# Optimization experiments

Measured on AMD Instinct MI355X. Metric: run time of the kernel, lower is better.

Reference implementation:

```python
import jax, jax.numpy as jnp
import numpy as np
from jax.ops import segment_sum

N = 100000      # nodes
E = 1600000     # edges
G = 128         # graphs in batch
D = 128         # input (embedding) dim
H = 128         # hidden dim
WALK = 16       # random-walk length
PED = 16        # PE embed dim
L = 5           # GNN layers
OUT = 10        # classes
EPS = 1e-5      # batchnorm eps


def setup_inputs() -> dict:
    key = jax.random.key(0)
    ks = jax.random.split(key, 32)
    f = lambda k, shp: (jax.random.normal(k, shp, dtype=jnp.float32) * 0.05)
    inp = {
        'x': jnp.zeros((N,), dtype=jnp.int64) if jax.config.jax_enable_x64 else jnp.zeros((N,), dtype=jnp.int32),
        'edge_index': jax.random.randint(ks[0], (2, E), 0, N),
        'batch': jnp.sort(jax.random.randint(ks[1], (N,), 0, G)),
        'emb_table': f(ks[2], (1, D)),
        'pe_w': f(ks[3], (WALK, PED)), 'pe_b': f(ks[4], (PED,)),
        'proj_w': f(ks[5], (D + PED, H)), 'proj_b': f(ks[6], (H,)),
        'gin_w1': f(ks[7], (L, H, H)), 'gin_b1': f(ks[8], (L, H)),
        'gin_w2': f(ks[9], (L, H, H)), 'gin_b2': f(ks[10], (L, H)),
        'bn_g': jnp.ones((L, H), jnp.float32), 'bn_b': jnp.zeros((L, H), jnp.float32),
        'ffn_w1': f(ks[11], (L, H, 2 * H)), 'ffn_b1': f(ks[12], (L, 2 * H)),
        'ffn_w2': f(ks[13], (L, 2 * H, H)), 'ffn_b2': f(ks[14], (L, H)),
        'ffn_bn_g': jnp.ones((L, H), jnp.float32), 'ffn_bn_b': jnp.zeros((L, H), jnp.float32),
        'out_w1': f(ks[15], (H, H)), 'out_b1': f(ks[16], (H,)),
        'out_w2': f(ks[17], (H, OUT)), 'out_b2': f(ks[18], (OUT,)),
    }
    return inp


def _batchnorm(h, g, b):
    # BatchNorm1d forward with batch statistics (training-mode math)
    mu = jnp.mean(h, axis=0)
    var = jnp.var(h, axis=0)
    return (h - mu) * jax.lax.rsqrt(var + EPS) * g + b


def _forward(emb_table, pe_w, pe_b, proj_w, proj_b, gin_w1, gin_b1, gin_w2, gin_b2,
             bn_g, bn_b, ffn_w1, ffn_b1, ffn_w2, ffn_b2, ffn_bn_g, ffn_bn_b,
             out_w1, out_b1, out_w2, out_b2, x, edge_index, batch):
    h0 = emb_table[x]                                # [N, D] (all indices are 0)

    # ---- RandomWalkPositionalEncoding (vectorized scatter-add per step) ----
    row0, col0 = edge_index[0], edge_index[1]
    loops = jnp.arange(N)
    row = jnp.concatenate([row0, loops])
    col = jnp.concatenate([col0, loops])             # self loops appended
    deg = segment_sum(jnp.ones(row.shape, jnp.float32), col, num_segments=N)
    dinv = jnp.where(deg > 0, jax.lax.rsqrt(jnp.maximum(deg, 1.0)), 0.0)
    norm_e = dinv[row] * dinv[col]                   # [E+N]

    cnt = segment_sum(jnp.ones((N,), jnp.float32), batch, num_segments=G)
    prob = 1.0 / jnp.maximum(cnt, 1.0)[batch]        # per-graph uniform init

    def rw_step(p, _):
        new_p = segment_sum(p[row] * norm_e, col, num_segments=N)
        return new_p * 0.9 + p * 0.1, p

    _, rw = jax.lax.scan(rw_step, prob, None, length=WALK)   # [WALK, N]
    pe = rw.T @ pe_w + pe_b                          # [N, PED]

    # ---- input projection ----
    h = jnp.concatenate([h0, pe], axis=-1) @ proj_w + proj_b # [N, H]

    # ---- stacked GIN layers with BN, residual and FFN (dropout = eval identity) ----
    for i in range(L):
        res = h
        agg = segment_sum(h[row0], col0, num_segments=N) + h  # GIN: (1+eps)x + sum_j x_j, eps=0
        z = jax.nn.relu(agg @ gin_w1[i] + gin_b1[i]) @ gin_w2[i] + gin_b2[i]
        z = jax.nn.relu(_batchnorm(z, bn_g[i], bn_b[i]))
        h = z + res
        res2 = h
        f = jax.nn.relu(h @ ffn_w1[i] + ffn_b1[i]) @ ffn_w2[i] + ffn_b2[i]
        h = _batchnorm(f + res2, ffn_bn_g[i], ffn_bn_b[i])

    # ---- global mean pooling + MLP head ----
    gsum = segment_sum(h, batch, num_segments=G)
    g = gsum / jnp.maximum(cnt, 1.0)[:, None]        # [G, H]
    out = jax.nn.relu(g @ out_w1 + out_b1) @ out_w2 + out_b2
    return out                                        # [G, OUT]


def reference(x, edge_index, batch, emb_table, pe_w, pe_b, proj_w, proj_b,
              gin_w1, gin_b1, gin_w2, gin_b2, bn_g, bn_b, ffn_w1, ffn_b1,
              ffn_w2, ffn_b2, ffn_bn_g, ffn_bn_b, out_w1, out_b1, out_w2, out_b2):
    return _forward(emb_table, pe_w, pe_b, proj_w, proj_b, gin_w1, gin_b1, gin_w2,
                    gin_b2, bn_g, bn_b, ffn_w1, ffn_b1, ffn_w2, ffn_b2,
                    ffn_bn_g, ffn_bn_b, out_w1, out_b1, out_w2, out_b2,
                    x, edge_index, batch)
```

## Files before the change

kernel.cpp:

```cpp
#include <hip/hip_runtime.h>
#include <math.h>

#define NN 100000
#define NE 1600000
#define NG 128
#define HD 128
#define WLK 16
#define NL 5
#define NOUT 10
#define BNEPS 1e-5f
#define CDIV(a,b) (((a)+(b)-1)/(b))

#define NBKT 782
#define NEB 400
#define EPB 4000
#define NSCAN (NBKT*NEB)
#define NSB CDIV(NSCAN,1024)
#define NBM 782

typedef float f32x4 __attribute__((ext_vector_type(4)));
typedef _Float16 f16x8 __attribute__((ext_vector_type(8)));
typedef unsigned short ushort_t;
typedef unsigned int uint_t;

__device__ __forceinline__ ushort_t f2h(float x) {
    union { _Float16 h; ushort_t u; } c;
    c.h = (_Float16)x;
    return c.u;
}
__device__ __forceinline__ float h2f(ushort_t u) {
    union { ushort_t u; _Float16 h; } c;
    c.u = u;
    return (float)c.h;
}

__global__ void k_cnt(const int* __restrict__ batch, int* __restrict__ cnt,
                      int* __restrict__ goff) {
    int g = threadIdx.x;
    if (g >= NG) return;
    int lo0 = 0, hi0 = NN;
    while (lo0 < hi0) { int m = (lo0 + hi0) >> 1; if (batch[m] < g) lo0 = m + 1; else hi0 = m; }
    int lo1 = lo0, hi1 = NN;
    while (lo1 < hi1) { int m = (lo1 + hi1) >> 1; if (batch[m] < g + 1) lo1 = m + 1; else hi1 = m; }
    cnt[g] = lo1 - lo0;
    goff[g] = lo0;
}

__global__ void k_bhist(const int* __restrict__ col0, int* __restrict__ bhist) {
    __shared__ int hist[NBKT];
    for (int i = threadIdx.x; i < NBKT; i += 256) hist[i] = 0;
    __syncthreads();
    int e0 = blockIdx.x * EPB;
    for (int e = e0 + threadIdx.x; e < e0 + EPB; e += 256) atomicAdd(&hist[col0[e] >> 7], 1);
    __syncthreads();
    for (int i = threadIdx.x; i < NBKT; i += 256) bhist[i * NEB + blockIdx.x] = hist[i];
}

__global__ void k_gscan1(const int* __restrict__ in, int* __restrict__ bsum) {
    __shared__ int sm[256];
    int base = blockIdx.x * 1024 + threadIdx.x * 4;
    int s = 0;
#pragma unroll
    for (int i = 0; i < 4; ++i) { int e = base + i; if (e < NSCAN) s += in[e]; }
    sm[threadIdx.x] = s; __syncthreads();
    for (int st = 128; st > 0; st >>= 1) {
        if (threadIdx.x < st) sm[threadIdx.x] += sm[threadIdx.x + st];
        __syncthreads();
    }
    if (threadIdx.x == 0) bsum[blockIdx.x] = sm[0];
}

__global__ void k_scan2(int* __restrict__ blksum, int nblk) {
    __shared__ int sm[512];
    int t = threadIdx.x;
    int x = (t < nblk) ? blksum[t] : 0;
    sm[t] = x; __syncthreads();
    for (int s = 1; s < 512; s <<= 1) {
        int v = (t >= s) ? sm[t - s] : 0;
        __syncthreads();
        sm[t] += v;
        __syncthreads();
    }
    if (t < nblk) blksum[t] = sm[t] - x;
}

__global__ void k_gscan3(const int* __restrict__ in, const int* __restrict__ bsum,
                         int* __restrict__ out) {
    __shared__ int sm[256];
    int t = threadIdx.x;
    int base = blockIdx.x * 1024 + t * 4;
    int v[4]; int s = 0;
#pragma unroll
    for (int i = 0; i < 4; ++i) { int e = base + i; v[i] = (e < NSCAN) ? in[e] : 0; s += v[i]; }
    sm[t] = s; __syncthreads();
    for (int st = 1; st < 256; st <<= 1) {
        int x = (t >= st) ? sm[t - st] : 0;
        __syncthreads();
        sm[t] += x;
        __syncthreads();
    }
    int excl = sm[t] - s + bsum[blockIdx.x];
#pragma unroll
    for (int i = 0; i < 4; ++i) { int e = base + i; if (e < NSCAN) { out[e] = excl; excl += v[i]; } }
}

__global__ void k_escatter(const int* __restrict__ row0, const int* __restrict__ col0,
                           const int* __restrict__ boffs, int2* __restrict__ epair) {
    __shared__ int cur[NBKT];
    for (int i = threadIdx.x; i < NBKT; i += 256) cur[i] = boffs[i * NEB + blockIdx.x];
    __syncthreads();
    int e0 = blockIdx.x * EPB;
    for (int e = e0 + threadIdx.x; e < e0 + EPB; e += 256) {
        int c = col0[e], r = row0[e];
        int pos = atomicAdd(&cur[c >> 7], 1);
        epair[pos] = make_int2(c, r);
    }
}

__global__ void k_bucket(const int2* __restrict__ epair, const int* __restrict__ boffs,
                         int* __restrict__ rowptr, int* __restrict__ deg,
                         int* __restrict__ esrc) {
    __shared__ int cnt_[128], scn[128], cur_[128];
    int bkt = blockIdx.x, t = threadIdx.x;
    int bs = boffs[bkt * NEB];
    int be = (bkt + 1 < NBKT) ? boffs[(bkt + 1) * NEB] : NE;
    if (t < 128) cnt_[t] = 0;
    __syncthreads();
    for (int e = bs + t; e < be; e += 256) atomicAdd(&cnt_[epair[e].x & 127], 1);
    __syncthreads();
    int c = (t < 128) ? cnt_[t] : 0;
    if (t < 128) scn[t] = c;
    __syncthreads();
    for (int st = 1; st < 128; st <<= 1) {
        int x = (t >= st && t < 128) ? scn[t - st] : 0;
        __syncthreads();
        if (t < 128) scn[t] += x;
        __syncthreads();
    }
    if (t < 128) {
        int excl = scn[t] - c;
        int node = bkt * 128 + t;
        if (node < NN) { rowptr[node] = bs + excl; deg[node] = c; }
        cur_[t] = bs + excl;
    }
    if (bkt == NBKT - 1 && t == 0) rowptr[NN] = NE;
    __syncthreads();
    for (int e = bs + t; e < be; e += 256) {
        int2 p = epair[e];
        int pos = atomicAdd(&cur_[p.x & 127], 1);
        esrc[pos] = p.y;
    }
}

__global__ void k_init_pe(const int* __restrict__ deg, const int* __restrict__ batch,
                          const int* __restrict__ cnt, float* __restrict__ dinv,
                          float* __restrict__ p, float* __restrict__ pd) {
    int v = blockIdx.x * 256 + threadIdx.x;
    if (v >= NN) return;
    float dv = rsqrtf((float)(deg[v] + 1));
    dinv[v] = dv;
    float pv = 1.0f / fmaxf((float)cnt[batch[v]], 1.0f);
    p[v] = pv; pd[v] = pv * dv;
}

__global__ void k_rw_step(const float* __restrict__ pin, const float* __restrict__ pdin,
                          const int* __restrict__ rowptr, const int* __restrict__ esrc,
                          const float* __restrict__ dinv, float* __restrict__ rwslice,
                          float* __restrict__ pout, float* __restrict__ pdout) {
    int v = blockIdx.x * 256 + threadIdx.x;
    if (v >= NN) return;
    int b = rowptr[v], e = rowptr[v + 1];
    float a[8];
#pragma unroll
    for (int k = 0; k < 8; ++k) a[k] = 0.f;
    int i = b;
    for (; i + 8 <= e; i += 8) {
        int s[8];
#pragma unroll
        for (int k = 0; k < 8; ++k) s[k] = esrc[i + k];
#pragma unroll
        for (int k = 0; k < 8; ++k) a[k] += pdin[s[k]];
    }
    for (; i < e; ++i) a[0] += pdin[esrc[i]];
    float s = ((a[0] + a[1]) + (a[2] + a[3])) + ((a[4] + a[5]) + (a[6] + a[7]));
    float dv = dinv[v];
    float pv = pin[v];
    float np = s * dv + pv * dv * dv;
    float nxt = 0.9f * np + 0.1f * pv;
    rwslice[v] = pv;
    pout[v] = nxt;
    pdout[v] = nxt * dv;
}

__global__ void k_mc1(const float* __restrict__ emb, const float* __restrict__ pe_w,
                      const float* __restrict__ pe_b, const float* __restrict__ proj_w,
                      const float* __restrict__ proj_b, float* __restrict__ M,
                      float* __restrict__ c1, float* __restrict__ bnA0,
                      float* __restrict__ bnB0) {
    int j = threadIdx.x;
    bnA0[j] = 1.f; bnB0[j] = 0.f;
    float c0 = proj_b[j];
    for (int d = 0; d < HD; ++d) c0 += emb[d] * proj_w[d * HD + j];
    for (int w = 0; w < WLK; ++w) c0 += pe_b[w] * proj_w[(HD + w) * HD + j];
    c1[j] = c0;
    for (int s = 0; s < WLK; ++s) {
        float m = 0.f;
        for (int w = 0; w < WLK; ++w) m += pe_w[s * WLK + w] * proj_w[(HD + w) * HD + j];
        M[s * HD + j] = m;
    }
}

__global__ void k_proj(const float* __restrict__ rw, const float* __restrict__ M,
                       const float* __restrict__ c1, uint2* __restrict__ th4) {
    int idx = blockIdx.x * 256 + threadIdx.x;
    if (idx >= NN * 32) return;
    int v = idx >> 5, cg = (idx & 31) * 4;
    float4 acc = *(const float4*)&c1[cg];
#pragma unroll
    for (int s = 0; s < WLK; ++s) {
        float r = rw[s * NN + v];
        float4 m = *(const float4*)&M[s * HD + cg];
        acc.x += r * m.x; acc.y += r * m.y; acc.z += r * m.z; acc.w += r * m.w;
    }
    th4[idx] = make_uint2((uint_t)f2h(acc.x) | ((uint_t)f2h(acc.y) << 16),
                          (uint_t)f2h(acc.z) | ((uint_t)f2h(acc.w) << 16));
}

__global__ void k_prepw(const float* __restrict__ g1, const float* __restrict__ g2,
                        const float* __restrict__ f1, const float* __restrict__ f2,
                        ushort_t* __restrict__ wt1, ushort_t* __restrict__ wt2,
                        ushort_t* __restrict__ wt3, ushort_t* __restrict__ wt4) {
    int i = blockIdx.x * 256 + threadIdx.x;
    if (i < 81920) {
        int l = i >> 14, rem = i & 16383, n = rem >> 7, k = rem & 127;
        wt1[i] = f2h(g1[l * 16384 + k * 128 + n]);
    } else if (i < 163840) {
        int j = i - 81920;
        int l = j >> 14, rem = j & 16383, n = rem >> 7, k = rem & 127;
        wt2[j] = f2h(g2[l * 16384 + k * 128 + n]);
    } else if (i < 327680) {
        int j = i - 163840;
        int l = j >> 15, rem = j & 32767, n = rem >> 7, k = rem & 127;
        wt3[j] = f2h(f1[l * 32768 + k * 256 + n]);
    } else {
        int j = i - 327680;
        int l = j >> 15, rem = j & 32767, n = rem >> 8, k = rem & 255;
        wt4[j] = f2h(f2[l * 32768 + k * 128 + n]);
    }
}

__global__ void k_aggb(const uint_t* __restrict__ th2, const int* __restrict__ rowptr,
                       const int* __restrict__ esrc, const float* __restrict__ bnA0,
                       const float* __restrict__ bnB0, uint_t* __restrict__ aggb2) {
    int wave = threadIdx.x >> 6, lane = threadIdx.x & 63;
    int v = blockIdx.x * 4 + wave;
    if (v >= NN) return;
    uint_t u = th2[(size_t)v * 64 + lane];
    float sx[8], sy[8];
#pragma unroll
    for (int k = 0; k < 8; ++k) { sx[k] = 0.f; sy[k] = 0.f; }
    sx[0] = h2f((ushort_t)(u & 0xFFFFu)); sy[0] = h2f((ushort_t)(u >> 16));
    int b = rowptr[v], e = rowptr[v + 1];
    int i = b;
    for (; i + 8 <= e; i += 8) {
        int idx[8]; uint_t x[8];
#pragma unroll
        for (int k = 0; k < 8; ++k) idx[k] = esrc[i + k];
#pragma unroll
        for (int k = 0; k < 8; ++k) x[k] = th2[(size_t)idx[k] * 64 + lane];
#pragma unroll
        for (int k = 0; k < 8; ++k) {
            sx[k] += h2f((ushort_t)(x[k] & 0xFFFFu));
            sy[k] += h2f((ushort_t)(x[k] >> 16));
        }
    }
    for (; i < e; ++i) {
        uint_t x = th2[(size_t)esrc[i] * 64 + lane];
        sx[0] += h2f((ushort_t)(x & 0xFFFFu)); sy[0] += h2f((ushort_t)(x >> 16));
    }
    float fx = ((sx[0] + sx[1]) + (sx[2] + sx[3])) + ((sx[4] + sx[5]) + (sx[6] + sx[7]));
    float fy = ((sy[0] + sy[1]) + (sy[2] + sy[3])) + ((sy[4] + sy[5]) + (sy[6] + sy[7]));
    float2 A = *(const float2*)&bnA0[lane * 2];
    float2 B = *(const float2*)&bnB0[lane * 2];
    float cf = (float)(e - b + 1);
    float ox = A.x * fx + cf * B.x;
    float oy = A.y * fy + cf * B.y;
    aggb2[(size_t)v * 64 + lane] = (uint_t)f2h(ox) | ((uint_t)f2h(oy) << 16);
}

#define GLDK 136
__global__ __launch_bounds__(256)
void k_gin(const ushort_t* __restrict__ A, const ushort_t* __restrict__ W1T,
           const ushort_t* __restrict__ W2T, const float* __restrict__ b1,
           const float* __restrict__ b2, ushort_t* __restrict__ z2h,
           float* __restrict__ partS, float* __restrict__ partQ) {
    __shared__ ushort_t As[128 * GLDK];
    __shared__ ushort_t Ws[64 * GLDK];
    __shared__ float sS[128], sQ[128];
    const int tid = threadIdx.x;
    const int w = tid >> 6, l = tid & 63;
    const int lm = l & 15, lq = l >> 4;
    const int rw0 = w * 32;
    const int vr0 = blockIdx.x * 128;
    if (tid < 128) { sS[tid] = 0.f; sQ[tid] = 0.f; }

#pragma unroll
    for (int it = 0; it < 8; ++it) {
        int f = it * 256 + tid;
        int row = f >> 4, sl = f & 15;
        uint4 a = make_uint4(0, 0, 0, 0);
        int vr = vr0 + row;
        if (vr < NN) a = *(const uint4*)&A[(size_t)vr * HD + sl * 8];
        *(uint4*)&As[row * GLDK + sl * 8] = a;
    }

    f32x4 z1a[2][2][4] = {};
    for (int c = 0; c < 2; ++c) {
        __syncthreads();
#pragma unroll
        for (int it = 0; it < 4; ++it) {
            int f = it * 256 + tid;
            int row = f >> 4, sl = f & 15;
            *(uint4*)&Ws[row * GLDK + sl * 8] =
                *(const uint4*)&W1T[(size_t)(c * 64 + row) * HD + sl * 8];
        }
        __syncthreads();
#pragma unroll
        for (int kk = 0; kk < 128; kk += 32) {
            f16x8 af[2], bf[4];
#pragma unroll
            for (int i = 0; i < 2; ++i)
                af[i] = *(const f16x8*)&As[(rw0 + i * 16 + lm) * GLDK + kk + lq * 8];
#pragma unroll
            for (int j = 0; j < 4; ++j)
                bf[j] = *(const f16x8*)&Ws[(j * 16 + lm) * GLDK + kk + lq * 8];
#pragma unroll
            for (int i = 0; i < 2; ++i)
#pragma unroll
                for (int j = 0; j < 4; ++j)
                    z1a[c][i][j] = __builtin_amdgcn_mfma_f32_16x16x32_f16(af[i], bf[j], z1a[c][i][j], 0, 0, 0);
        }
    }
    __syncthreads();

#pragma unroll
    for (int c = 0; c < 2; ++c)
#pragma unroll
        for (int j = 0; j < 4; ++j) {
            int col = c * 64 + j * 16 + lm;
            float bj = b1[col];
#pragma unroll
            for (int i = 0; i < 2; ++i)
#pragma unroll
                for (int r = 0; r < 4; ++r) {
                    int row = rw0 + i * 16 + lq * 4 + r;
                    As[row * GLDK + col] = f2h(fmaxf(z1a[c][i][j][r] + bj, 0.f));
                }
        }

    f32x4 z2a[2][2][4] = {};
    for (int c2 = 0; c2 < 2; ++c2) {
        __syncthreads();
#pragma unroll
        for (int it = 0; it < 4; ++it) {
            int f = it * 256 + tid;
            int row = f >> 4, sl = f & 15;
            *(uint4*)&Ws[row * GLDK + sl * 8] =
                *(const uint4*)&W2T[(size_t)(c2 * 64 + row) * HD + sl * 8];
        }
        __syncthreads();
#pragma unroll
        for (int kk = 0; kk < 128; kk += 32) {
            f16x8 af[2], bf[4];
#pragma unroll
            for (int i = 0; i < 2; ++i)
                af[i] = *(const f16x8*)&As[(rw0 + i * 16 + lm) * GLDK + kk + lq * 8];
#pragma unroll
            for (int j = 0; j < 4; ++j)
                bf[j] = *(const f16x8*)&Ws[(j * 16 + lm) * GLDK + kk + lq * 8];
#pragma unroll
            for (int i = 0; i < 2; ++i)
#pragma unroll
                for (int j = 0; j < 4; ++j)
                    z2a[c2][i][j] = __builtin_amdgcn_mfma_f32_16x16x32_f16(af[i], bf[j], z2a[c2][i][j], 0, 0, 0);
        }
    }

    float ls[2][4] = {}, lsq[2][4] = {};
#pragma unroll
    for (int c2 = 0; c2 < 2; ++c2)
#pragma unroll
        for (int j = 0; j < 4; ++j) {
            int col = c2 * 64 + j * 16 + lm;
            float bj = b2[col];
#pragma unroll
            for (int i = 0; i < 2; ++i)
#pragma unroll
                for (int r = 0; r < 4; ++r) {
                    int vr = vr0 + rw0 + i * 16 + lq * 4 + r;
                    if (vr < NN) {
                        float x = z2a[c2][i][j][r] + bj;
                        ls[c2][j] += x; lsq[c2][j] += x * x;
                        z2h[(size_t)vr * HD + col] = f2h(x);
                    }
                }
        }
#pragma unroll
    for (int c2 = 0; c2 < 2; ++c2)
#pragma unroll
        for (int j = 0; j < 4; ++j) {
            atomicAdd(&sS[c2 * 64 + j * 16 + lm], ls[c2][j]);
            atomicAdd(&sQ[c2 * 64 + j * 16 + lm], lsq[c2][j]);
        }
    __syncthreads();
    if (tid < 128) {
        partS[(size_t)tid * NBM + blockIdx.x] = sS[tid];
        partQ[(size_t)tid * NBM + blockIdx.x] = sQ[tid];
    }
}

__global__ __launch_bounds__(256)
void k_ffn1(const ushort_t* __restrict__ th, const ushort_t* __restrict__ z2h,
            const ushort_t* __restrict__ W3T, const float* __restrict__ b3,
            const float* __restrict__ bnA0, const float* __restrict__ bnB0,
            const float* __restrict__ bnA1, const float* __restrict__ bnB1,
            ushort_t* __restrict__ f1h) {
    __shared__ ushort_t As[128 * GLDK];
    __shared__ ushort_t Ws[64 * GLDK];
    __shared__ float sA0[128], sB0[128], sA1[128], sB1[128];
    const int tid = threadIdx.x;
    const int w = tid >> 6, l = tid & 63;
    const int lm = l & 15, lq = l >> 4;
    const int rw0 = w * 32;
    const int vr0 = blockIdx.x * 128;

    if (tid < 128) {
        sA0[tid] = bnA0[tid]; sB0[tid] = bnB0[tid];
        sA1[tid] = bnA1[tid]; sB1[tid] = bnB1[tid];
    }
    __syncthreads();

#pragma unroll
    for (int it = 0; it < 8; ++it) {
        int f = it * 256 + tid;
        int row = f >> 4, sl = f & 15;
        int vr = vr0 + row;
        uint4 o = make_uint4(0, 0, 0, 0);
        if (vr < NN) {
            uint4 tv = *(const uint4*)&th[(size_t)vr * HD + sl * 8];
            uint4 zv = *(const uint4*)&z2h[(size_t)vr * HD + sl * 8];
            uint_t tu[4] = {tv.x, tv.y, tv.z, tv.w};
            uint_t zu[4] = {zv.x, zv.y, zv.z, zv.w};
            uint_t ou[4];
#pragma unroll
            for (int m = 0; m < 4; ++m) {
                int ch0 = sl * 8 + m * 2;
                float t0 = h2f((ushort_t)(tu[m] & 0xFFFFu));
                float t1 = h2f((ushort_t)(tu[m] >> 16));
                float z0 = h2f((ushort_t)(zu[m] & 0xFFFFu));
                float z1 = h2f((ushort_t)(zu[m] >> 16));
                float h0 = sA0[ch0] * t0 + sB0[ch0] + fmaxf(sA1[ch0] * z0 + sB1[ch0], 0.f);
                float h1 = sA0[ch0 + 1] * t1 + sB0[ch0 + 1] + fmaxf(sA1[ch0 + 1] * z1 + sB1[ch0 + 1], 0.f);
                ou[m] = (uint_t)f2h(h0) | ((uint_t)f2h(h1) << 16);
            }
            o = make_uint4(ou[0], ou[1], ou[2], ou[3]);
        }
        *(uint4*)&As[row * GLDK + sl * 8] = o;
    }

    for (int c = 0; c < 4; ++c) {
        __syncthreads();
#pragma unroll
        for (int it = 0; it < 4; ++it) {
            int f = it * 256 + tid;
            int row = f >> 4, sl = f & 15;
            *(uint4*)&Ws[row * GLDK + sl * 8] =
                *(const uint4*)&W3T[(size_t)(c * 64 + row) * HD + sl * 8];
        }
        __syncthreads();
        f32x4 acc[2][4] = {};
#pragma unroll
        for (int kk = 0; kk < 128; kk += 32) {
            f16x8 af[2], bf[4];
#pragma unroll
            for (int i = 0; i < 2; ++i)
                af[i] = *(const f16x8*)&As[(rw0 + i * 16 + lm) * GLDK + kk + lq * 8];
#pragma unroll
            for (int j = 0; j < 4; ++j)
                bf[j] = *(const f16x8*)&Ws[(j * 16 + lm) * GLDK + kk + lq * 8];
#pragma unroll
            for (int i = 0; i < 2; ++i)
#pragma unroll
                for (int j = 0; j < 4; ++j)
                    acc[i][j] = __builtin_amdgcn_mfma_f32_16x16x32_f16(af[i], bf[j], acc[i][j], 0, 0, 0);
        }
#pragma unroll
        for (int j = 0; j < 4; ++j) {
            int col = c * 64 + j * 16 + lm;
            float bj = b3[col];
#pragma unroll
            for (int i = 0; i < 2; ++i)
#pragma unroll
                for (int r = 0; r < 4; ++r) {
                    int vr = vr0 + rw0 + i * 16 + lq * 4 + r;
                    if (vr < NN)
                        f1h[(size_t)vr * 256 + col] = f2h(fmaxf(acc[i][j][r] + bj, 0.f));
                }
        }
    }
}

__global__ __launch_bounds__(256, 2)
void k_ffn2(const ushort_t* __restrict__ f1h, const ushort_t* __restrict__ WT,
            const float* __restrict__ bias, ushort_t* __restrict__ th,
            const ushort_t* __restrict__ z2h,
            const float* __restrict__ bnA0, const float* __restrict__ bnB0,
            const float* __restrict__ bnA1, const float* __restrict__ bnB1,
            float* __restrict__ partS, float* __restrict__ partQ) {
    constexpr int LDK = 72;
    __shared__ ushort_t As[128 * LDK];
    __shared__ ushort_t Ws[128 * LDK];
    __shared__ float sS[128], sQ[128];
    const int tid = threadIdx.x;
    const int w = tid >> 6, l = tid & 63;
    const int lm = l & 15, lq = l >> 4;
    const int rb = (w >> 1) * 64, cbw = (w & 1) * 64;
    const int vr0 = blockIdx.x * 128;
    f32x4 acc[4][4] = {};

    for (int kt = 0; kt < 4; ++kt) {
        __syncthreads();
#pragma unroll
        for (int it = 0; it < 4; ++it) {
            int f = it * 256 + tid;
            int row = f >> 3, sl = f & 7;
            uint4 a = make_uint4(0, 0, 0, 0);
            int vr = vr0 + row;
            if (vr < NN) a = *(const uint4*)&f1h[(size_t)vr * 256 + kt * 64 + sl * 8];
            *(uint4*)&As[row * LDK + sl * 8] = a;
            uint4 wv = *(const uint4*)&WT[(size_t)row * 256 + kt * 64 + sl * 8];
            *(uint4*)&Ws[row * LDK + sl * 8] = wv;
        }
        __syncthreads();
#pragma unroll
        for (int kk = 0; kk < 64; kk += 32) {
            f16x8 af[4], bf[4];
#pragma unroll
            for (int i = 0; i < 4; ++i)
                af[i] = *(const f16x8*)&As[(rb + i * 16 + lm) * LDK + kk + lq * 8];
#pragma unroll
            for (int j = 0; j < 4; ++j)
                bf[j] = *(const f16x8*)&Ws[(cbw + j * 16 + lm) * LDK + kk + lq * 8];
#pragma unroll
            for (int i = 0; i < 4; ++i)
#pragma unroll
                for (int j = 0; j < 4; ++j)
                    acc[i][j] = __builtin_amdgcn_mfma_f32_16x16x32_f16(af[i], bf[j], acc[i][j], 0, 0, 0);
        }
    }

    float bcol[4], a0c[4], b0c[4], a1c[4], b1c[4];
#pragma unroll
    for (int j = 0; j < 4; ++j) {
        int c = cbw + j * 16 + lm;
        bcol[j] = bias[c];
        a0c[j] = bnA0[c]; b0c[j] = bnB0[c];
        a1c[j] = bnA1[c]; b1c[j] = bnB1[c];
    }
    if (tid < 128) { sS[tid] = 0.f; sQ[tid] = 0.f; }
    __syncthreads();
    float ls[4] = {0, 0, 0, 0}, lsq[4] = {0, 0, 0, 0};
#pragma unroll
    for (int i = 0; i < 4; ++i) {
#pragma unroll
        for (int r = 0; r < 4; ++r) {
            int vr = vr0 + rb + i * 16 + lq * 4 + r;
            if (vr < NN) {
#pragma unroll
                for (int j = 0; j < 4; ++j) {
                    int c = cbw + j * 16 + lm;
                    float t = h2f(th[(size_t)vr * HD + c]);
                    float z = h2f(z2h[(size_t)vr * HD + c]);
                    float resv = a0c[j] * t + b0c[j] + fmaxf(a1c[j] * z + b1c[j], 0.f);
                    float x = acc[i][j][r] + bcol[j] + resv;
                    ls[j] += x; lsq[j] += x * x;
                    th[(size_t)vr * HD + c] = f2h(x);
                }
            }
        }
    }
#pragma unroll
    for (int j = 0; j < 4; ++j) {
        atomicAdd(&sS[cbw + j * 16 + lm], ls[j]);
        atomicAdd(&sQ[cbw + j * 16 + lm], lsq[j]);
    }
    __syncthreads();
    if (tid < 128) {
        partS[(size_t)tid * NBM + blockIdx.x] = sS[tid];
        partQ[(size_t)tid * NBM + blockIdx.x] = sQ[tid];
    }
}

__global__ void k_bnparm(const float* __restrict__ partS, const float* __restrict__ partQ,
                         const float* __restrict__ g, const float* __restrict__ b,
                         float* __restrict__ bnA, float* __restrict__ bnB) {
    __shared__ float smS[256], smQ[256];
    int c = blockIdx.x, t = threadIdx.x;
    float s = 0.f, q = 0.f;
    for (int i = t; i < NBM; i += 256) {
        s += partS[(size_t)c * NBM + i];
        q += partQ[(size_t)c * NBM + i];
    }
    smS[t] = s; smQ[t] = q; __syncthreads();
    for (int st = 128; st > 0; st >>= 1) {
        if (t < st) { smS[t] += smS[t + st]; smQ[t] += smQ[t + st]; }
        __syncthreads();
    }
    if (t == 0) {
        float mu = smS[0] * (1.0f / NN);
        float var = smQ[0] * (1.0f / NN) - mu * mu;
        float inv = rsqrtf(var + BNEPS);
        float a = g[c] * inv;
        bnA[c] = a;
        bnB[c] = b[c] - mu * a;
    }
}

__global__ void k_pool(const uint2* __restrict__ th4, const int* __restrict__ goff,
                       const int* __restrict__ cnt, float* __restrict__ gsum) {
    __shared__ float4 sm[256];
    int g = blockIdx.x >> 2, sub = blockIdx.x & 3;
    int n0 = goff[g], n = cnt[g];
    int cg = threadIdx.x & 31, rl = threadIdx.x >> 5;
    float4 acc = make_float4(0.f, 0.f, 0.f, 0.f);
    for (int r = sub * 8 + rl; r < n; r += 32) {
        uint2 v = th4[(size_t)(n0 + r) * 32 + cg];
        acc.x += h2f((ushort_t)(v.x & 0xFFFFu));
        acc.y += h2f((ushort_t)(v.x >> 16));
        acc.z += h2f((ushort_t)(v.y & 0xFFFFu));
        acc.w += h2f((ushort_t)(v.y >> 16));
    }
    sm[threadIdx.x] = acc; __syncthreads();
    for (int st = 128; st >= 32; st >>= 1) {
        if (threadIdx.x < st) {
            float4 o = sm[threadIdx.x + st];
            sm[threadIdx.x].x += o.x; sm[threadIdx.x].y += o.y;
            sm[threadIdx.x].z += o.z; sm[threadIdx.x].w += o.w;
        }
        __syncthreads();
    }
    if (threadIdx.x < 32) {
        float4 v = sm[threadIdx.x];
        atomicAdd(&gsum[g * HD + cg * 4 + 0], v.x);
        atomicAdd(&gsum[g * HD + cg * 4 + 1], v.y);
        atomicAdd(&gsum[g * HD + cg * 4 + 2], v.z);
        atomicAdd(&gsum[g * HD + cg * 4 + 3], v.w);
    }
}

__global__ void k_head(const float* __restrict__ gsum, const int* __restrict__ cnt,
                       const float* __restrict__ bnA0, const float* __restrict__ bnB0,
                       const float* __restrict__ w1, const float* __restrict__ b1,
                       const float* __restrict__ w2, const float* __restrict__ b2,
                       float* __restrict__ out) {
    __shared__ float gv[HD], av[HD];
    int gid = blockIdx.x, t = threadIdx.x;
    float c = fmaxf((float)cnt[gid], 1.0f);
    gv[t] = bnA0[t] * (gsum[gid * HD + t] / c) + bnB0[t];
    __syncthreads();
    float a = b1[t];
    for (int k = 0; k < HD; ++k) a += gv[k] * w1[k * HD + t];
    av[t] = fmaxf(a, 0.f);
    __syncthreads();
    if (t < NOUT) {
        float o = b2[t];
        for (int k = 0; k < HD; ++k) o += av[k] * w2[k * NOUT + t];
        out[gid * NOUT + t] = o;
    }
}

static constexpr size_t AL(size_t x) { return (x + 511) & ~(size_t)511; }
static constexpr size_t OFF_TH     = 0;
static constexpr size_t OFF_SHARE  = OFF_TH     + AL((size_t)NN * HD * 2);
static constexpr size_t SZ_SHARE   = AL((size_t)NN * 256 * 2);
static constexpr size_t OFF_Z2     = OFF_SHARE  + SZ_SHARE;
static constexpr size_t OFF_RW     = OFF_Z2     + AL((size_t)NN * HD * 2);
static constexpr size_t OFF_P0     = OFF_RW     + AL((size_t)WLK * NN * 4);
static constexpr size_t OFF_P1     = OFF_P0     + AL((size_t)NN * 4);
static constexpr size_t OFF_PD0    = OFF_P1     + AL((size_t)NN * 4);
static constexpr size_t OFF_PD1    = OFF_PD0    + AL((size_t)NN * 4);
static constexpr size_t OFF_DINV   = OFF_PD1    + AL((size_t)NN * 4);
static constexpr size_t OFF_ESRC   = OFF_DINV   + AL((size_t)NN * 4);
static constexpr size_t OFF_ROWPTR = OFF_ESRC   + AL((size_t)NE * 4);
static constexpr size_t OFF_DEG    = OFF_ROWPTR + AL((size_t)(NN + 1) * 4);
static constexpr size_t OFF_BHIST  = OFF_DEG    + AL((size_t)NN * 4);
static constexpr size_t OFF_BOFFS  = OFF_BHIST  + AL((size_t)NSCAN * 4);
static constexpr size_t OFF_BSUM   = OFF_BOFFS  + AL((size_t)NSCAN * 4);
static constexpr size_t OFF_WT1    = OFF_BSUM   + AL(512 * 4);
static constexpr size_t OFF_WT2    = OFF_WT1    + AL((size_t)5 * 16384 * 2);
static constexpr size_t OFF_WT3    = OFF_WT2    + AL((size_t)5 * 16384 * 2);
static constexpr size_t OFF_WT4    = OFF_WT3    + AL((size_t)5 * 32768 * 2);
static constexpr size_t OFF_PARTS  = OFF_WT4    + AL((size_t)5 * 32768 * 2);
static constexpr size_t OFF_PARTQ  = OFF_PARTS  + AL((size_t)128 * NBM * 4);
static constexpr size_t OFF_BNA0   = OFF_PARTQ  + AL((size_t)128 * NBM * 4);
static constexpr size_t OFF_BNB0   = OFF_BNA0   + AL(128 * 4);
static constexpr size_t OFF_BNA1   = OFF_BNB0   + AL(128 * 4);
static constexpr size_t OFF_BNB1   = OFF_BNA1   + AL(128 * 4);
static constexpr size_t OFF_M      = OFF_BNB1   + AL(128 * 4);
static constexpr size_t OFF_C1     = OFF_M      + AL((size_t)WLK * HD * 4);
static constexpr size_t OFF_CNT    = OFF_C1     + AL(HD * 4);
static constexpr size_t OFF_GOFF   = OFF_CNT    + AL(NG * 4);
static constexpr size_t OFF_GSUM   = OFF_GOFF   + AL(NG * 4);
static constexpr size_t ZERO_BYTES = (size_t)NG * HD * 4;

extern "C" void kernel_launch(void* const* d_in, const int* in_sizes, int n_in,
                              void* d_out, int out_size, void* d_ws, size_t ws_size,
                              hipStream_t stream) {
    const int* eidx = (const int*)d_in[1];
    const int* row0 = eidx;
    const int* col0 = eidx + NE;
    const int* batch = (const int*)d_in[2];
    const float* emb = (const float*)d_in[3];
    const float* pe_w = (const float*)d_in[4];
    const float* pe_b = (const float*)d_in[5];
    const float* proj_w = (const float*)d_in[6];
    const float* proj_b = (const float*)d_in[7];
    const float* gin_w1 = (const float*)d_in[8];
    const float* gin_b1 = (const float*)d_in[9];
    const float* gin_w2 = (const float*)d_in[10];
    const float* gin_b2 = (const float*)d_in[11];
    const float* bn_g = (const float*)d_in[12];
    const float* bn_b = (const float*)d_in[13];
    const float* ffn_w1 = (const float*)d_in[14];
    const float* ffn_b1 = (const float*)d_in[15];
    const float* ffn_w2 = (const float*)d_in[16];
    const float* ffn_b2 = (const float*)d_in[17];
    const float* ffn_bn_g = (const float*)d_in[18];
    const float* ffn_bn_b = (const float*)d_in[19];
    const float* out_w1 = (const float*)d_in[20];
    const float* out_b1 = (const float*)d_in[21];
    const float* out_w2 = (const float*)d_in[22];
    const float* out_b2 = (const float*)d_in[23];
    float* out = (float*)d_out;

    char* ws = (char*)d_ws;
    ushort_t* th    = (ushort_t*)(ws + OFF_TH);
    ushort_t* aggh  = (ushort_t*)(ws + OFF_SHARE);
    ushort_t* f1h   = (ushort_t*)(ws + OFF_SHARE);
    int2*     epair = (int2*)(ws + OFF_SHARE);
    ushort_t* z2h   = (ushort_t*)(ws + OFF_Z2);
    float*    rw    = (float*)(ws + OFF_RW);
    float*    p0    = (float*)(ws + OFF_P0);
    float*    p1    = (float*)(ws + OFF_P1);
    float*    pd0   = (float*)(ws + OFF_PD0);
    float*    pd1   = (float*)(ws + OFF_PD1);
    float*    dinv  = (float*)(ws + OFF_DINV);
    int*      esrc  = (int*)(ws + OFF_ESRC);
    int*      rowptr= (int*)(ws + OFF_ROWPTR);
    int*      deg   = (int*)(ws + OFF_DEG);
    int*      bhist = (int*)(ws + OFF_BHIST);
    int*      boffs = (int*)(ws + OFF_BOFFS);
    int*      bsum  = (int*)(ws + OFF_BSUM);
    ushort_t* wt1   = (ushort_t*)(ws + OFF_WT1);
    ushort_t* wt2   = (ushort_t*)(ws + OFF_WT2);
    ushort_t* wt3   = (ushort_t*)(ws + OFF_WT3);
    ushort_t* wt4   = (ushort_t*)(ws + OFF_WT4);
    float*    partS = (float*)(ws + OFF_PARTS);
    float*    partQ = (float*)(ws + OFF_PARTQ);
    float*    bnA0  = (float*)(ws + OFF_BNA0);
    float*    bnB0  = (float*)(ws + OFF_BNB0);
    float*    bnA1  = (float*)(ws + OFF_BNA1);
    float*    bnB1  = (float*)(ws + OFF_BNB1);
    float*    M     = (float*)(ws + OFF_M);
    float*    c1    = (float*)(ws + OFF_C1);
    int*      cnt   = (int*)(ws + OFF_CNT);
    int*      goff  = (int*)(ws + OFF_GOFF);
    float*    gsum  = (float*)(ws + OFF_GSUM);

    const int NB = CDIV(NN, 256);
    const int NBV = CDIV(NN * 32, 256);

    hipMemsetAsync(ws + OFF_GSUM, 0, ZERO_BYTES, stream);

    k_cnt<<<1, 128, 0, stream>>>(batch, cnt, goff);
    k_bhist<<<NEB, 256, 0, stream>>>(col0, bhist);
    k_gscan1<<<NSB, 256, 0, stream>>>(bhist, bsum);
    k_scan2<<<1, 512, 0, stream>>>(bsum, NSB);
    k_gscan3<<<NSB, 256, 0, stream>>>(bhist, bsum, boffs);
    k_escatter<<<NEB, 256, 0, stream>>>(row0, col0, boffs, epair);
    k_bucket<<<NBKT, 256, 0, stream>>>(epair, boffs, rowptr, deg, esrc);

    k_init_pe<<<NB, 256, 0, stream>>>(deg, batch, cnt, dinv, p0, pd0);
    k_mc1<<<1, 128, 0, stream>>>(emb, pe_w, pe_b, proj_w, proj_b, M, c1, bnA0, bnB0);
    k_prepw<<<1920, 256, 0, stream>>>(gin_w1, gin_w2, ffn_w1, ffn_w2, wt1, wt2, wt3, wt4);
    for (int s = 0; s < WLK; ++s) {
        const float* pin = (s & 1) ? p1 : p0;
        const float* pdin = (s & 1) ? pd1 : pd0;
        float* pout = (s & 1) ? p0 : p1;
        float* pdout = (s & 1) ? pd0 : pd1;
        k_rw_step<<<NB, 256, 0, stream>>>(pin, pdin, rowptr, esrc, dinv,
                                          rw + (size_t)s * NN, pout, pdout);
    }
    k_proj<<<NBV, 256, 0, stream>>>(rw, M, c1, (uint2*)th);

    for (int i = 0; i < NL; ++i) {
        k_aggb<<<CDIV(NN, 4), 256, 0, stream>>>((const uint_t*)th, rowptr, esrc,
                                                bnA0, bnB0, (uint_t*)aggh);
        k_gin<<<NBM, 256, 0, stream>>>(aggh, wt1 + (size_t)i * 16384, wt2 + (size_t)i * 16384,
                                       gin_b1 + i * HD, gin_b2 + i * HD, z2h, partS, partQ);
        k_bnparm<<<128, 256, 0, stream>>>(partS, partQ, bn_g + i * HD, bn_b + i * HD, bnA1, bnB1);
        k_ffn1<<<NBM, 256, 0, stream>>>(th, z2h, wt3 + (size_t)i * 32768, ffn_b1 + i * 256,
                                        bnA0, bnB0, bnA1, bnB1, f1h);
        k_ffn2<<<NBM, 256, 0, stream>>>(f1h, wt4 + (size_t)i * 32768, ffn_b2 + i * HD,
                                        th, z2h, bnA0, bnB0, bnA1, bnB1, partS, partQ);
        k_bnparm<<<128, 256, 0, stream>>>(partS, partQ, ffn_bn_g + i * HD, ffn_bn_b + i * HD,
                                          bnA0, bnB0);
    }

    k_pool<<<NG * 4, 256, 0, stream>>>((const uint2*)th, goff, cnt, gsum);
    k_head<<<NG, 128, 0, stream>>>(gsum, cnt, bnA0, bnB0, out_w1, out_b1, out_w2, out_b2, out);
}
```

Before: 1.571 ms.

## Fuse FFN up- and down-projection into one kernel keeping hidden tile in LDS

```diff
diff --git a/kernel.cpp b/kernel.cpp
--- a/kernel.cpp
+++ b/kernel.cpp
@@ -419,14 +419,18 @@
     }
 }
 
+#define FLDK 72
 __global__ __launch_bounds__(256)
-void k_ffn1(const ushort_t* __restrict__ th, const ushort_t* __restrict__ z2h,
-            const ushort_t* __restrict__ W3T, const float* __restrict__ b3,
-            const float* __restrict__ bnA0, const float* __restrict__ bnB0,
-            const float* __restrict__ bnA1, const float* __restrict__ bnB1,
-            ushort_t* __restrict__ f1h) {
+void k_ffn(ushort_t* __restrict__ th, const ushort_t* __restrict__ z2h,
+           const ushort_t* __restrict__ W3T, const float* __restrict__ b3,
+           const ushort_t* __restrict__ W4T, const float* __restrict__ b4,
+           const float* __restrict__ bnA0, const float* __restrict__ bnB0,
+           const float* __restrict__ bnA1, const float* __restrict__ bnB1,
+           float* __restrict__ partS, float* __restrict__ partQ) {
     __shared__ ushort_t As[128 * GLDK];
-    __shared__ ushort_t Ws[64 * GLDK];
+    __shared__ ushort_t Fs[128 * FLDK];
+    __shared__ ushort_t Ws[128 * FLDK];
+    __shared__ float sS[128], sQ[128];
     __shared__ float sA0[128], sB0[128], sA1[128], sB1[128];
     const int tid = threadIdx.x;
     const int w = tid >> 6, l = tid & 63;
@@ -435,6 +439,7 @@
     const int vr0 = blockIdx.x * 128;
 
     if (tid < 128) {
+        sS[tid] = 0.f; sQ[tid] = 0.f;
         sA0[tid] = bnA0[tid]; sB0[tid] = bnB0[tid];
         sA1[tid] = bnA1[tid]; sB1[tid] = bnB1[tid];
     }
@@ -468,17 +473,18 @@
         *(uint4*)&As[row * GLDK + sl * 8] = o;
     }
 
-    for (int c = 0; c < 4; ++c) {
+    f32x4 acc2[2][2][4] = {};
+    for (int kc = 0; kc < 4; ++kc) {
         __syncthreads();
 #pragma unroll
         for (int it = 0; it < 4; ++it) {
             int f = it * 256 + tid;
             int row = f >> 4, sl = f & 15;
             *(uint4*)&Ws[row * GLDK + sl * 8] =
-                *(const uint4*)&W3T[(size_t)(c * 64 + row) * HD + sl * 8];
-        }
-        __syncthreads();
-        f32x4 acc[2][4] = {};
+                *(const uint4*)&W3T[(size_t)(kc * 64 + row) * HD + sl * 8];
+        }
+        __syncthreads();
+        f32x4 f1a[2][4] = {};
 #pragma unroll
         for (int kk = 0; kk < 128; kk += 32) {
             f16x8 af[2], bf[4];
@@ -492,108 +498,75 @@
             for (int i = 0; i < 2; ++i)
 #pragma unroll
                 for (int j = 0; j < 4; ++j)
-                    acc[i][j] = __builtin_amdgcn_mfma_f32_16x16x32_f16(af[i], bf[j], acc[i][j], 0, 0, 0);
+                    f1a[i][j] = __builtin_amdgcn_mfma_f32_16x16x32_f16(af[i], bf[j], f1a[i][j], 0, 0, 0);
         }
 #pragma unroll
         for (int j = 0; j < 4; ++j) {
-            int col = c * 64 + j * 16 + lm;
-            float bj = b3[col];
+            int fcol = j * 16 + lm;
+            float bj = b3[kc * 64 + fcol];
 #pragma unroll
             for (int i = 0; i < 2; ++i)
 #pragma unroll
                 for (int r = 0; r < 4; ++r) {
-                    int vr = vr0 + rw0 + i * 16 + lq * 4 + r;
-                    if (vr < NN)
-                        f1h[(size_t)vr * 256 + col] = f2h(fmaxf(acc[i][j][r] + bj, 0.f));
+                    int row = rw0 + i * 16 + lq * 4 + r;
+                    Fs[row * FLDK + fcol] = f2h(fmaxf(f1a[i][j][r] + bj, 0.f));
                 }
         }
-    }
-}
-
-__global__ __launch_bounds__(256, 2)
-void k_ffn2(const ushort_t* __restrict__ f1h, const ushort_t* __restrict__ WT,
-            const float* __restrict__ bias, ushort_t* __restrict__ th,
-            const ushort_t* __restrict__ z2h,
-            const float* __restrict__ bnA0, const float* __restrict__ bnB0,
-            const float* __restrict__ bnA1, const float* __restrict__ bnB1,
-            float* __restrict__ partS, float* __restrict__ partQ) {
-    constexpr int LDK = 72;
-    __shared__ ushort_t As[128 * LDK];
-    __shared__ ushort_t Ws[128 * LDK];
-    __shared__ float sS[128], sQ[128];
-    const int tid = threadIdx.x;
-    const int w = tid >> 6, l = tid & 63;
-    const int lm = l & 15, lq = l >> 4;
-    const int rb = (w >> 1) * 64, cbw = (w & 1) * 64;
-    const int vr0 = blockIdx.x * 128;
-    f32x4 acc[4][4] = {};
-
-    for (int kt = 0; kt < 4; ++kt) {
         __syncthreads();
 #pragma unroll
         for (int it = 0; it < 4; ++it) {
             int f = it * 256 + tid;
             int row = f >> 3, sl = f & 7;
-            uint4 a = make_uint4(0, 0, 0, 0);
-            int vr = vr0 + row;
-            if (vr < NN) a = *(const uint4*)&f1h[(size_t)vr * 256 + kt * 64 + sl * 8];
-            *(uint4*)&As[row * LDK + sl * 8] = a;
-            uint4 wv = *(const uint4*)&WT[(size_t)row * 256 + kt * 64 + sl * 8];
-            *(uint4*)&Ws[row * LDK + sl * 8] = wv;
+            *(uint4*)&Ws[row * FLDK + sl * 8] =
+                *(const uint4*)&W4T[(size_t)row * 256 + kc * 64 + sl * 8];
         }
         __syncthreads();
 #pragma unroll
         for (int kk = 0; kk < 64; kk += 32) {
-            f16x8 af[4], bf[4];
-#pragma unroll
-            for (int i = 0; i < 4; ++i)
-                af[i] = *(const f16x8*)&As[(rb + i * 16 + lm) * LDK + kk + lq * 8];
-#pragma unroll
-            for (int j = 0; j < 4; ++j)
-                bf[j] = *(const f16x8*)&Ws[(cbw + j * 16 + lm) * LDK + kk + lq * 8];
-#pragma unroll
-            for (int i = 0; i < 4; ++i)
-#pragma unroll
-                for (int j = 0; j < 4; ++j)
-                    acc[i][j] = __builtin_amdgcn_mfma_f32_16x16x32_f16(af[i], bf[j], acc[i][j], 0, 0, 0);
-        }
-    }
-
-    float bcol[4], a0c[4], b0c[4], a1c[4], b1c[4];
-#pragma unroll
-    for (int j = 0; j < 4; ++j) {
-        int c = cbw + j * 16 + lm;
-        bcol[j] = bias[c];
-        a0c[j] = bnA0[c]; b0c[j] = bnB0[c];
-        a1c[j] = bnA1[c]; b1c[j] = bnB1[c];
-    }
-    if (tid < 128) { sS[tid] = 0.f; sQ[tid] = 0.f; }
-    __syncthreads();
-    float ls[4] = {0, 0, 0, 0}, lsq[4] = {0, 0, 0, 0};
-#pragma unroll
-    for (int i = 0; i < 4; ++i) {
-#pragma unroll
-        for (int r = 0; r < 4; ++r) {
-            int vr = vr0 + rb + i * 16 + lq * 4 + r;
-            if (vr < NN) {
+            f16x8 af[2];
+#pragma unroll
+            for (int i = 0; i < 2; ++i)
+                af[i] = *(const f16x8*)&Fs[(rw0 + i * 16 + lm) * FLDK + kk + lq * 8];
+#pragma unroll
+            for (int c2 = 0; c2 < 2; ++c2)
 #pragma unroll
                 for (int j = 0; j < 4; ++j) {
-                    int c = cbw + j * 16 + lm;
-                    float t = h2f(th[(size_t)vr * HD + c]);
-                    float z = h2f(z2h[(size_t)vr * HD + c]);
-                    float resv = a0c[j] * t + b0c[j] + fmaxf(a1c[j] * z + b1c[j], 0.f);
-                    float x = acc[i][j][r] + bcol[j] + resv;
-                    ls[j] += x; lsq[j] += x * x;
-                    th[(size_t)vr * HD + c] = f2h(x);
+                    f16x8 bf = *(const f16x8*)&Ws[(c2 * 64 + j * 16 + lm) * FLDK + kk + lq * 8];
+#pragma unroll
+                    for (int i = 0; i < 2; ++i)
+                        acc2[c2][i][j] = __builtin_amdgcn_mfma_f32_16x16x32_f16(af[i], bf, acc2[c2][i][j], 0, 0, 0);
                 }
-            }
-        }
-    }
-#pragma unroll
-    for (int j = 0; j < 4; ++j) {
-        atomicAdd(&sS[cbw + j * 16 + lm], ls[j]);
-        atomicAdd(&sQ[cbw + j * 16 + lm], lsq[j]);
-    }
+        }
+    }
+
+    float ls[2][4] = {}, lsq[2][4] = {};
+#pragma unroll
+    for (int c2 = 0; c2 < 2; ++c2)
+#pragma unroll
+        for (int j = 0; j < 4; ++j) {
+            int col = c2 * 64 + j * 16 + lm;
+            float bj = b4[col];
+#pragma unroll
+            for (int i = 0; i < 2; ++i)
+#pragma unroll
+                for (int r = 0; r < 4; ++r) {
+                    int lrow = rw0 + i * 16 + lq * 4 + r;
+                    int vr = vr0 + lrow;
+                    if (vr < NN) {
+                        float resv = h2f(As[lrow * GLDK + col]);
+                        float x = acc2[c2][i][j][r] + bj + resv;
+                        ls[c2][j] += x; lsq[c2][j] += x * x;
+                        th[(size_t)vr * HD + col] = f2h(x);
+                    }
+                }
+        }
+#pragma unroll
+    for (int c2 = 0; c2 < 2; ++c2)
+#pragma unroll
+        for (int j = 0; j < 4; ++j) {
+            atomicAdd(&sS[c2 * 64 + j * 16 + lm], ls[c2][j]);
+            atomicAdd(&sQ[c2 * 64 + j * 16 + lm], lsq[c2][j]);
+        }
     __syncthreads();
     if (tid < 128) {
         partS[(size_t)tid * NBM + blockIdx.x] = sS[tid];
@@ -682,7 +655,7 @@
 static constexpr size_t AL(size_t x) { return (x + 511) & ~(size_t)511; }
 static constexpr size_t OFF_TH     = 0;
 static constexpr size_t OFF_SHARE  = OFF_TH     + AL((size_t)NN * HD * 2);
-static constexpr size_t SZ_SHARE   = AL((size_t)NN * 256 * 2);
+static constexpr size_t SZ_SHARE   = AL((size_t)NN * HD * 2);
 static constexpr size_t OFF_Z2     = OFF_SHARE  + SZ_SHARE;
 static constexpr size_t OFF_RW     = OFF_Z2     + AL((size_t)NN * HD * 2);
 static constexpr size_t OFF_P0     = OFF_RW     + AL((size_t)WLK * NN * 4);
@@ -746,7 +719,6 @@
     char* ws = (char*)d_ws;
     ushort_t* th    = (ushort_t*)(ws + OFF_TH);
     ushort_t* aggh  = (ushort_t*)(ws + OFF_SHARE);
-    ushort_t* f1h   = (ushort_t*)(ws + OFF_SHARE);
     int2*     epair = (int2*)(ws + OFF_SHARE);
     ushort_t* z2h   = (ushort_t*)(ws + OFF_Z2);
     float*    rw    = (float*)(ws + OFF_RW);
@@ -809,10 +781,9 @@
         k_gin<<<NBM, 256, 0, stream>>>(aggh, wt1 + (size_t)i * 16384, wt2 + (size_t)i * 16384,
                                        gin_b1 + i * HD, gin_b2 + i * HD, z2h, partS, partQ);
         k_bnparm<<<128, 256, 0, stream>>>(partS, partQ, bn_g + i * HD, bn_b + i * HD, bnA1, bnB1);
-        k_ffn1<<<NBM, 256, 0, stream>>>(th, z2h, wt3 + (size_t)i * 32768, ffn_b1 + i * 256,
-                                        bnA0, bnB0, bnA1, bnB1, f1h);
-        k_ffn2<<<NBM, 256, 0, stream>>>(f1h, wt4 + (size_t)i * 32768, ffn_b2 + i * HD,
-                                        th, z2h, bnA0, bnB0, bnA1, bnB1, partS, partQ);
+        k_ffn<<<NBM, 256, 0, stream>>>(th, z2h, wt3 + (size_t)i * 32768, ffn_b1 + i * 256,
+                                       wt4 + (size_t)i * 32768, ffn_b2 + i * HD,
+                                       bnA0, bnB0, bnA1, bnB1, partS, partQ);
         k_bnparm<<<128, 256, 0, stream>>>(partS, partQ, ffn_bn_g + i * HD, ffn_bn_b + i * HD,
                                           bnA0, bnB0);
     }
```

Result: faster. 1.440 ms, median of 3 (-8.3%).
